# Kernel optimization log

Hardware: AMD Instinct MI355X
Metric: run time of the kernel (lower is better)

## Reference

```python
import jax, jax.numpy as jnp
import numpy as np

# dims: M=512 new tokens, N=2048 model dim, D=128 head dim, H=16 heads,
# L=4096 cache length, P=2048 cache write offset

def setup_inputs() -> dict:
    key = jax.random.key(0)
    k0, k1, k2, k3 = jax.random.split(key, 4)
    M, N, D, L = 512, 2048, 128, 4096
    X = jax.random.normal(k0, (M, N), jnp.float32)
    # scale weights ~1/sqrt(N) so projections have unit-ish scale
    W_qkv = jax.random.normal(k1, (N, 3 * N), jnp.float32) * (N ** -0.5)
    H = N // D
    cache_K = jax.random.normal(k2, (H, L, D), jnp.float32)
    # realistic cache state: keys stored in cache are RMS-normalized
    cache_K = cache_K * jax.lax.rsqrt(jnp.mean(cache_K * cache_K, axis=-1, keepdims=True))
    cache_V = jax.random.normal(k3, (H, L, D), jnp.float32)
    return {"X": X, "W_qkv": W_qkv, "cache_K": cache_K, "cache_V": cache_V, "P": 2048}


def reference(X, W_qkv, cache_K, cache_V, P):
    M = X.shape[0]
    H, L, D = cache_K.shape
    qkv = X @ W_qkv                              # [M, 3N]
    q, k, v = jnp.split(qkv, 3, axis=-1)         # each [M, N]
    q = q.reshape(M, H, D).transpose(1, 0, 2)    # [H, M, D]
    k = k.reshape(M, H, D).transpose(1, 0, 2)
    v = v.reshape(M, H, D).transpose(1, 0, 2)
    # RMS-style normalization (no learned gain, no eps in original)
    q = q * jax.lax.rsqrt(jnp.mean(q * q, axis=-1, keepdims=True))
    k = k * jax.lax.rsqrt(jnp.mean(k * k, axis=-1, keepdims=True))
    # scatter-update into KV cache at position P
    Kc = jax.lax.dynamic_update_slice(cache_K, k, (0, P, 0))  # [H, L, D]
    Vc = jax.lax.dynamic_update_slice(cache_V, v, (0, P, 0))
    # unmasked, unscaled attention over the full cache (faithful to original:
    # plain exp/sum, no max-subtraction, no 1/sqrt(D))
    scores = jnp.einsum('hmd,hld->hml', q, Kc)   # [H, M, L]
    w = jnp.exp(scores)
    w = w / jnp.sum(w, axis=-1, keepdims=True)
    out = jnp.einsum('hml,hld->hmd', w, Vc)      # [H, M, D]
    return out.transpose(1, 0, 2).reshape(M, H * D)
```

## Files before the change

kernel.cpp:

```cpp
#include <hip/hip_runtime.h>
#include <math.h>

typedef _Float16 half_t;
typedef _Float16 half8 __attribute__((ext_vector_type(8)));
typedef _Float16 half4_t __attribute__((ext_vector_type(4)));
typedef _Float16 half2_t __attribute__((ext_vector_type(2)));
typedef float floatx4 __attribute__((ext_vector_type(4)));

#define M_TOK 512
#define N_DIM 2048
#define D_HEAD 128
#define H_HEADS 16
#define L_CACHE 4096
#define THREE_N 6144
#define NCHUNK 8
#define LCHUNK 512

__global__ __launch_bounds__(256) void prep_kernel(const float* __restrict__ W,
                                                   const float* __restrict__ X,
                                                   half_t* __restrict__ W16T,
                                                   half_t* __restrict__ X16) {
    __shared__ half_t tile[64 * 66];
    int b = blockIdx.x;
    int t = threadIdx.x;

    if (b < 3072) {
        int n0 = (b % 96) * 64, k0 = (b / 96) * 64;
        {
            int k = t >> 2, c0 = (t & 3) * 16;
            const float* src = W + (size_t)(k0 + k) * THREE_N + n0 + c0;
            float4 v[4];
#pragma unroll
            for (int j = 0; j < 4; ++j) v[j] = *(const float4*)(src + j * 4);
#pragma unroll
            for (int j = 0; j < 4; ++j) {
                tile[(c0 + j * 4 + 0) * 66 + k] = (half_t)v[j].x;
                tile[(c0 + j * 4 + 1) * 66 + k] = (half_t)v[j].y;
                tile[(c0 + j * 4 + 2) * 66 + k] = (half_t)v[j].z;
                tile[(c0 + j * 4 + 3) * 66 + k] = (half_t)v[j].w;
            }
        }
        __syncthreads();
        {
            int n = t >> 2, kg = (t & 3) * 16;
            half_t* dst = W16T + (size_t)(n0 + n) * N_DIM + k0 + kg;
            *(half8*)(dst) = *(half8*)&tile[n * 66 + kg];
            *(half8*)(dst + 8) = *(half8*)&tile[n * 66 + kg + 8];
        }
        return;
    }
    b -= 3072;
    {
        size_t i = (size_t)b * 2048 + t * 4;
        float4 v0 = *(const float4*)(X + i);
        float4 v1 = *(const float4*)(X + i + 1024);
        half4_t h0 = {(half_t)v0.x, (half_t)v0.y, (half_t)v0.z, (half_t)v0.w};
        half4_t h1 = {(half_t)v1.x, (half_t)v1.y, (half_t)v1.z, (half_t)v1.w};
        *(half4_t*)(X16 + i) = h0;
        *(half4_t*)(X16 + i + 1024) = h1;
    }
}

__global__ __launch_bounds__(256) void mega_kernel(const half_t* __restrict__ X16,
                                                   const half_t* __restrict__ W16T,
                                                   const float* __restrict__ cK,
                                                   const float* __restrict__ cV,
                                                   const int* __restrict__ Pp,
                                                   half_t* __restrict__ Q16,
                                                   half_t* __restrict__ K16,
                                                   half_t* __restrict__ V16T) {
    __shared__ __align__(16) char smem[46592];
    const int t = threadIdx.x;
    int b = blockIdx.x;

    if (b >= 384) {
        b -= 384;
        const int P = *Pp;
        if (b < 4096) {
            int l0 = (b & 255) * 16;
            if (l0 >= P && l0 + 16 <= P + M_TOK) return;
            size_t i = (size_t)b * 2048 + t * 4;
            int r0 = l0 + (t >> 5), r1 = r0 + 8;
            float4 v0 = *(const float4*)(cK + i);
            float4 v1 = *(const float4*)(cK + i + 1024);
            half4_t h0 = {(half_t)v0.x, (half_t)v0.y, (half_t)v0.z, (half_t)v0.w};
            half4_t h1 = {(half_t)v1.x, (half_t)v1.y, (half_t)v1.z, (half_t)v1.w};
            if (r0 < P || r0 >= P + M_TOK) *(half4_t*)(K16 + i) = h0;
            if (r1 < P || r1 >= P + M_TOK) *(half4_t*)(K16 + i + 1024) = h1;
            return;
        }
        b -= 4096;
        {
            int h = b >> 7;
            int rem = b & 127;
            int lt = rem >> 1, dt = rem & 1;
            int l0 = lt * 64, d0 = dt * 64;
            if (l0 >= P && l0 + 64 <= P + M_TOK) return;
            bool overlap = (l0 < P + M_TOK) && (l0 + 64 > P);
            half_t* tile = (half_t*)smem;
            {
                int l = t >> 2, c0 = (t & 3) * 16;
                const float* src = cV + ((size_t)h * L_CACHE + l0 + l) * D_HEAD + d0 + c0;
                float4 v[4];
#pragma unroll
                for (int j = 0; j < 4; ++j) v[j] = *(const float4*)(src + j * 4);
#pragma unroll
                for (int j = 0; j < 4; ++j) {
                    tile[(c0 + j * 4 + 0) * 66 + l] = (half_t)v[j].x;
                    tile[(c0 + j * 4 + 1) * 66 + l] = (half_t)v[j].y;
                    tile[(c0 + j * 4 + 2) * 66 + l] = (half_t)v[j].z;
                    tile[(c0 + j * 4 + 3) * 66 + l] = (half_t)v[j].w;
                }
            }
            __syncthreads();
            {
                int d = t >> 2, lg = (t & 3) * 16;
                half_t* dst = V16T + ((size_t)h * D_HEAD + d0 + d) * L_CACHE + l0 + lg;
                if (!overlap) {
                    *(half8*)(dst) = *(half8*)&tile[d * 66 + lg];
                    *(half8*)(dst + 8) = *(half8*)&tile[d * 66 + lg + 8];
                } else {
#pragma unroll
                    for (int j = 0; j < 16; ++j) {
                        int l = l0 + lg + j;
                        if (l < P || l >= P + M_TOK) dst[j] = tile[d * 66 + lg + j];
                    }
                }
            }
            return;
        }
    }

    half_t* As = (half_t*)smem;
    half_t* Bs = (half_t*)(smem + 9216);
    half_t* Vt = (half_t*)(smem + 27648);
    float* ssb = (float*)(smem + 46080);
    const int wid = t >> 6, lane = t & 63;
    const int quad = lane >> 4, ln = lane & 15;
    const int bx = b % 48, by = b / 48;
    const int m0 = by * 64, n0 = bx * 128;
    const int wm = (wid >> 1) * 32, wn = (wid & 1) * 64;

    floatx4 acc[2][4] = {};

    const int ar = t >> 3, ag = (t & 7) * 8;
    const int br = t >> 3, bg = (t & 7) * 8;

    for (int k0 = 0; k0 < N_DIM; k0 += 64) {
        __syncthreads();
#pragma unroll
        for (int p = 0; p < 2; ++p) {
            int r = ar + p * 32;
            *(half8*)&As[r * 72 + ag] =
                *(const half8*)(X16 + (size_t)(m0 + r) * N_DIM + k0 + ag);
        }
#pragma unroll
        for (int p = 0; p < 4; ++p) {
            int r = br + p * 32;
            *(half8*)&Bs[r * 72 + bg] =
                *(const half8*)(W16T + (size_t)(n0 + r) * N_DIM + k0 + bg);
        }
        __syncthreads();
#pragma unroll
        for (int kt = 0; kt < 2; ++kt) {
            half8 a[2], bb[4];
#pragma unroll
            for (int i = 0; i < 2; ++i)
                a[i] = *(half8*)&As[(wm + i * 16 + ln) * 72 + kt * 32 + quad * 8];
#pragma unroll
            for (int j = 0; j < 4; ++j)
                bb[j] = *(half8*)&Bs[(wn + j * 16 + ln) * 72 + kt * 32 + quad * 8];
#pragma unroll
            for (int i = 0; i < 2; ++i)
#pragma unroll
                for (int j = 0; j < 4; ++j)
                    acc[i][j] = __builtin_amdgcn_mfma_f32_16x16x32_f16(a[i], bb[j], acc[i][j], 0, 0, 0);
        }
    }

    const int seg = bx >> 4, h = bx & 15;
    const int P = *Pp;

    if (seg < 2) {
        float ss[2][4], scale[2][4];
#pragma unroll
        for (int i = 0; i < 2; ++i)
#pragma unroll
            for (int r = 0; r < 4; ++r) {
                float s = 0.f;
#pragma unroll
                for (int j = 0; j < 4; ++j) s += acc[i][j][r] * acc[i][j][r];
#pragma unroll
                for (int msk = 1; msk < 16; msk <<= 1) s += __shfl_xor(s, msk, 64);
                ss[i][r] = s;
            }
        if (ln == 0) {
#pragma unroll
            for (int i = 0; i < 2; ++i)
#pragma unroll
                for (int r = 0; r < 4; ++r)
                    ssb[wid * 32 + i * 16 + quad * 4 + r] = ss[i][r];
        }
        __syncthreads();
#pragma unroll
        for (int i = 0; i < 2; ++i)
#pragma unroll
            for (int r = 0; r < 4; ++r)
                scale[i][r] =
                    rsqrtf((ss[i][r] + ssb[(wid ^ 1) * 32 + i * 16 + quad * 4 + r]) * (1.0f / 128.0f));
#pragma unroll
        for (int i = 0; i < 2; ++i) {
            int mbase = m0 + wm + i * 16 + quad * 4;
#pragma unroll
            for (int j = 0; j < 4; ++j) {
                int col = wn + j * 16 + ln;
#pragma unroll
                for (int r = 0; r < 4; ++r) {
                    int m = mbase + r;
                    half_t val = (half_t)(acc[i][j][r] * scale[i][r]);
                    if (seg == 0)
                        Q16[((size_t)h * M_TOK + m) * D_HEAD + col] = val;
                    else
                        K16[((size_t)h * L_CACHE + P + m) * D_HEAD + col] = val;
                }
            }
        }
    } else {
#pragma unroll
        for (int i = 0; i < 2; ++i) {
            int mbase = wm + i * 16 + quad * 4;
#pragma unroll
            for (int j = 0; j < 4; ++j) {
                int d = wn + j * 16 + ln;
#pragma unroll
                for (int r = 0; r < 4; ++r)
                    Vt[d * 72 + mbase + r] = (half_t)acc[i][j][r];
            }
        }
        __syncthreads();
#pragma unroll
        for (int p = 0; p < 4; ++p) {
            int s = p * 256 + t;
            int d = s >> 3, sg = s & 7;
            *(half8*)(V16T + ((size_t)h * D_HEAD + d) * L_CACHE + P + m0 + sg * 8) =
                *(half8*)&Vt[d * 72 + sg * 8];
        }
    }
}

__global__ __launch_bounds__(256, 4) void attn_partial_kernel(const half_t* __restrict__ Q16,
                                                              const half_t* __restrict__ K16,
                                                              const half_t* __restrict__ V16T,
                                                              half_t* __restrict__ Opart,
                                                              float* __restrict__ mstat,
                                                              float* __restrict__ lstat) {
    __shared__ half_t Ks[64 * 128];
    __shared__ half_t Vs[128 * 64];
    __shared__ half_t Ps[4 * 16 * 64];
    const int t = threadIdx.x, w = t >> 6, lane = t & 63;
    const int quad = lane >> 4, ln = lane & 15;

    const int bid = blockIdx.x;
    const int xcd = bid & 7, slot = bid >> 3;
    const int pair = (xcd << 4) | (slot >> 3);
    const int h = pair & 15, c = pair >> 4, mi = slot & 7;
    const int mb = mi * 64;

    const half_t* Qh = Q16 + (size_t)h * M_TOK * D_HEAD;
    const half_t* Kh = K16 + (size_t)h * L_CACHE * D_HEAD;
    const half_t* Vh = V16T + (size_t)h * D_HEAD * L_CACHE;

    const int m0 = mb + w * 16;
    half8 qf[4];
#pragma unroll
    for (int dt = 0; dt < 4; ++dt)
        qf[dt] = *(const half8*)(Qh + (size_t)(m0 + ln) * D_HEAD + dt * 32 + quad * 8);

    floatx4 oacc[8] = {};
    float mrow = -INFINITY;
    float lrow = 0.f;

    half_t* Pw = Ps + w * (16 * 64);
    const int psw = (ln & 7) << 3;

    const int l0base = c * LCHUNK;
    const int kr = t >> 4, kc = (t & 15) * 8;
    const int vr = t >> 3, vc = (t & 7) * 8;
    const int ksw = (kr & 7) << 3;
    const int vsw = (vr & 7) << 3;

    half8 kreg[4], vreg[4];
#pragma unroll
    for (int p = 0; p < 4; ++p) {
        kreg[p] = *(const half8*)(Kh + (size_t)(l0base + p * 16 + kr) * D_HEAD + kc);
        vreg[p] = *(const half8*)(Vh + (size_t)(p * 32 + vr) * L_CACHE + l0base + vc);
    }

    for (int it = 0; it < LCHUNK / 64; ++it) {
        __syncthreads();
#pragma unroll
        for (int p = 0; p < 4; ++p)
            *(half8*)&Ks[(p * 16 + kr) * 128 + (kc ^ ksw)] = kreg[p];
#pragma unroll
        for (int p = 0; p < 4; ++p)
            *(half8*)&Vs[(p * 32 + vr) * 64 + (vc ^ vsw)] = vreg[p];
        if (it + 1 < LCHUNK / 64) {
            int l1 = l0base + (it + 1) * 64;
#pragma unroll
            for (int p = 0; p < 4; ++p) {
                kreg[p] = *(const half8*)(Kh + (size_t)(l1 + p * 16 + kr) * D_HEAD + kc);
                vreg[p] = *(const half8*)(Vh + (size_t)(p * 32 + vr) * L_CACHE + l1 + vc);
            }
        }
        __syncthreads();

        floatx4 sacc[4] = {};
#pragma unroll
        for (int dt = 0; dt < 4; ++dt) {
            half8 kf[4];
#pragma unroll
            for (int nt = 0; nt < 4; ++nt)
                kf[nt] = *(half8*)&Ks[(nt * 16 + ln) * 128 + ((dt * 32 + quad * 8) ^ psw)];
#pragma unroll
            for (int nt = 0; nt < 4; ++nt)
                sacc[nt] = __builtin_amdgcn_mfma_f32_16x16x32_f16(kf[nt], qf[dt], sacc[nt], 0, 0, 0);
        }

        {
            float mx = sacc[0][0];
#pragma unroll
            for (int nt = 0; nt < 4; ++nt)
#pragma unroll
                for (int r = 0; r < 4; ++r) mx = fmaxf(mx, sacc[nt][r]);
            mx = fmaxf(mx, __shfl_xor(mx, 16));
            mx = fmaxf(mx, __shfl_xor(mx, 32));
            if (__ballot(mx > mrow)) {
                float mnew = fmaxf(mrow, mx);
                float alpha = __expf(mrow - mnew);
                mrow = mnew;
                lrow *= alpha;
                float ar[4];
#pragma unroll
                for (int r = 0; r < 4; ++r) ar[r] = __shfl(alpha, quad * 4 + r, 16);
#pragma unroll
                for (int nt8 = 0; nt8 < 8; ++nt8)
#pragma unroll
                    for (int r = 0; r < 4; ++r) oacc[nt8][r] *= ar[r];
            }
            float psum = 0.f;
#pragma unroll
            for (int nt = 0; nt < 4; ++nt) {
                half4_t h4;
#pragma unroll
                for (int r = 0; r < 4; ++r) {
                    float p = __expf(sacc[nt][r] - mrow);
                    psum += p;
                    h4[r] = (half_t)p;
                }
                *(half4_t*)&Pw[ln * 64 + ((nt * 16 + quad * 4) ^ psw)] = h4;
            }
            psum += __shfl_xor(psum, 16);
            psum += __shfl_xor(psum, 32);
            lrow += psum;
        }

#pragma unroll
        for (int kt = 0; kt < 2; ++kt) {
            half8 a = *(half8*)&Pw[ln * 64 + ((kt * 32 + quad * 8) ^ psw)];
#pragma unroll
            for (int nt8 = 0; nt8 < 8; ++nt8) {
                half8 b = *(half8*)&Vs[(nt8 * 16 + ln) * 64 + ((kt * 32 + quad * 8) ^ psw)];
                oacc[nt8] = __builtin_amdgcn_mfma_f32_16x16x32_f16(a, b, oacc[nt8], 0, 0, 0);
            }
        }
    }

    half_t* Oc = Opart + ((size_t)(c * H_HEADS + h) * M_TOK) * D_HEAD;
    float* ms = mstat + (size_t)(c * H_HEADS + h) * M_TOK;
    float* ls = lstat + (size_t)(c * H_HEADS + h) * M_TOK;
#pragma unroll
    for (int nt8 = 0; nt8 < 8; ++nt8) {
        int col = nt8 * 16 + ln;
#pragma unroll
        for (int r = 0; r < 4; ++r)
            Oc[(size_t)(m0 + quad * 4 + r) * D_HEAD + col] = (half_t)oacc[nt8][r];
    }
    if (lane < 16) {
        ms[m0 + lane] = mrow;
        ls[m0 + lane] = lrow;
    }
}

__global__ __launch_bounds__(256) void combine_kernel(const half_t* __restrict__ Opart,
                                                      const float* __restrict__ mstat,
                                                      const float* __restrict__ lstat,
                                                      float* __restrict__ out) {
    int gw = blockIdx.x * 4 + (threadIdx.x >> 6);
    int lane = threadIdx.x & 63;
    int h = gw >> 9, m = gw & 511;
    int d = lane * 2;

    float ms[NCHUNK];
    float mg = -INFINITY;
#pragma unroll
    for (int c = 0; c < NCHUNK; ++c) {
        ms[c] = mstat[((c * H_HEADS + h) << 9) + m];
        mg = fmaxf(mg, ms[c]);
    }
    float denom = 0.f, o0 = 0.f, o1 = 0.f;
#pragma unroll
    for (int c = 0; c < NCHUNK; ++c) {
        float e = __expf(ms[c] - mg);
        denom += lstat[((c * H_HEADS + h) << 9) + m] * e;
        const half_t* Oc = Opart + (((size_t)(c * H_HEADS + h) << 9) + m) * D_HEAD + d;
        half2_t v = *(const half2_t*)Oc;
        o0 += (float)v.x * e;
        o1 += (float)v.y * e;
    }
    float inv = 1.0f / denom;
    float* op = out + (size_t)m * N_DIM + h * D_HEAD + d;
    op[0] = o0 * inv;
    op[1] = o1 * inv;
}

extern "C" void kernel_launch(void* const* d_in, const int* in_sizes, int n_in,
                              void* d_out, int out_size, void* d_ws, size_t ws_size,
                              hipStream_t stream) {
    const float* X = (const float*)d_in[0];
    const float* W = (const float*)d_in[1];
    const float* cK = (const float*)d_in[2];
    const float* cV = (const float*)d_in[3];
    const int* Pp = (const int*)d_in[4];
    float* out = (float*)d_out;

    char* ws = (char*)d_ws;
    half_t* Q16 = (half_t*)(ws + 0);
    half_t* K16 = (half_t*)(ws + 2097152);
    half_t* V16T = (half_t*)(ws + 18874368);
    half_t* X16 = (half_t*)(ws + 35651584);
    half_t* W16T = (half_t*)(ws + 37748736);
    half_t* Opart = (half_t*)(ws + 37748736);
    float* mstat = (float*)(ws + 71303168);
    float* lstat = (float*)(ws + 71827456);

    prep_kernel<<<3584, 256, 0, stream>>>(W, X, W16T, X16);
    mega_kernel<<<6528, 256, 0, stream>>>(X16, W16T, cK, cV, Pp, Q16, K16, V16T);
    attn_partial_kernel<<<1024, 256, 0, stream>>>(Q16, K16, V16T, Opart, mstat, lstat);
    combine_kernel<<<2048, 256, 0, stream>>>(Opart, mstat, lstat, out);
}
```

Baseline: 212.4 us.

## Fuse split-L combine into attention kernel via last-block atomic counter

Removes the separate combine kernel launch. Each attention block bumps an atomic counter for its (head, m-block) group, and the last of the eight chunk blocks to finish merges all partial outputs and writes the final result. This saves one kernel launch and its tail. In exchange the last-arriving blocks run a serial tail, and a hipMemsetAsync is added to reset the counters.

```diff
diff --git a/kernel.cpp b/kernel.cpp
--- a/kernel.cpp
+++ b/kernel.cpp
@@ -253,10 +253,13 @@
                                                               const half_t* __restrict__ V16T,
                                                               half_t* __restrict__ Opart,
                                                               float* __restrict__ mstat,
-                                                              float* __restrict__ lstat) {
+                                                              float* __restrict__ lstat,
+                                                              float* __restrict__ out,
+                                                              int* __restrict__ cnt) {
     __shared__ half_t Ks[64 * 128];
     __shared__ half_t Vs[128 * 64];
     __shared__ half_t Ps[4 * 16 * 64];
+    __shared__ int lastS;
     const int t = threadIdx.x, w = t >> 6, lane = t & 63;
     const int quad = lane >> 4, ln = lane & 15;
 
@@ -339,13 +342,13 @@
                 float alpha = __expf(mrow - mnew);
                 mrow = mnew;
                 lrow *= alpha;
-                float ar[4];
-#pragma unroll
-                for (int r = 0; r < 4; ++r) ar[r] = __shfl(alpha, quad * 4 + r, 16);
+                float ar4[4];
+#pragma unroll
+                for (int r = 0; r < 4; ++r) ar4[r] = __shfl(alpha, quad * 4 + r, 16);
 #pragma unroll
                 for (int nt8 = 0; nt8 < 8; ++nt8)
 #pragma unroll
-                    for (int r = 0; r < 4; ++r) oacc[nt8][r] *= ar[r];
+                    for (int r = 0; r < 4; ++r) oacc[nt8][r] *= ar4[r];
             }
             float psum = 0.f;
 #pragma unroll
@@ -389,38 +392,49 @@
         ms[m0 + lane] = mrow;
         ls[m0 + lane] = lrow;
     }
-}
-
-__global__ __launch_bounds__(256) void combine_kernel(const half_t* __restrict__ Opart,
-                                                      const float* __restrict__ mstat,
-                                                      const float* __restrict__ lstat,
-                                                      float* __restrict__ out) {
-    int gw = blockIdx.x * 4 + (threadIdx.x >> 6);
-    int lane = threadIdx.x & 63;
-    int h = gw >> 9, m = gw & 511;
-    int d = lane * 2;
-
-    float ms[NCHUNK];
-    float mg = -INFINITY;
-#pragma unroll
-    for (int c = 0; c < NCHUNK; ++c) {
-        ms[c] = mstat[((c * H_HEADS + h) << 9) + m];
-        mg = fmaxf(mg, ms[c]);
-    }
-    float denom = 0.f, o0 = 0.f, o1 = 0.f;
-#pragma unroll
-    for (int c = 0; c < NCHUNK; ++c) {
-        float e = __expf(ms[c] - mg);
-        denom += lstat[((c * H_HEADS + h) << 9) + m] * e;
-        const half_t* Oc = Opart + (((size_t)(c * H_HEADS + h) << 9) + m) * D_HEAD + d;
-        half2_t v = *(const half2_t*)Oc;
-        o0 += (float)v.x * e;
-        o1 += (float)v.y * e;
-    }
-    float inv = 1.0f / denom;
-    float* op = out + (size_t)m * N_DIM + h * D_HEAD + d;
-    op[0] = o0 * inv;
-    op[1] = o1 * inv;
+
+    __syncthreads();
+    if (t == 0) {
+        int prev = __hip_atomic_fetch_add(&cnt[h * 8 + mi], 1, __ATOMIC_ACQ_REL,
+                                          __HIP_MEMORY_SCOPE_AGENT);
+        int last = (prev == NCHUNK - 1) ? 1 : 0;
+        if (last) {
+            __hip_atomic_store(&cnt[h * 8 + mi], 0, __ATOMIC_RELAXED,
+                               __HIP_MEMORY_SCOPE_AGENT);
+            __builtin_amdgcn_fence(__ATOMIC_ACQUIRE, "agent");
+        }
+        lastS = last;
+    }
+    __syncthreads();
+    if (lastS) {
+#pragma unroll 1
+        for (int rr = w; rr < 64; rr += 4) {
+            int m = mb + rr;
+            int d = lane * 2;
+            float msv[NCHUNK];
+            float mg = -INFINITY;
+#pragma unroll
+            for (int cc = 0; cc < NCHUNK; ++cc) {
+                msv[cc] = mstat[((cc * H_HEADS + h) << 9) + m];
+                mg = fmaxf(mg, msv[cc]);
+            }
+            float denom = 0.f, o0 = 0.f, o1 = 0.f;
+#pragma unroll
+            for (int cc = 0; cc < NCHUNK; ++cc) {
+                float e = __expf(msv[cc] - mg);
+                denom += lstat[((cc * H_HEADS + h) << 9) + m] * e;
+                const half_t* Oc2 =
+                    Opart + (((size_t)(cc * H_HEADS + h) << 9) + m) * D_HEAD + d;
+                half2_t v = *(const half2_t*)Oc2;
+                o0 += (float)v.x * e;
+                o1 += (float)v.y * e;
+            }
+            float inv = 1.0f / denom;
+            float* op = out + (size_t)m * N_DIM + h * D_HEAD + d;
+            op[0] = o0 * inv;
+            op[1] = o1 * inv;
+        }
+    }
 }
 
 extern "C" void kernel_launch(void* const* d_in, const int* in_sizes, int n_in,
@@ -442,9 +456,11 @@
     half_t* Opart = (half_t*)(ws + 37748736);
     float* mstat = (float*)(ws + 71303168);
     float* lstat = (float*)(ws + 71827456);
-
+    int* cnt = (int*)(ws + 72089600);
+
+    hipMemsetAsync(cnt, 0, 512, stream);
     prep_kernel<<<3584, 256, 0, stream>>>(W, X, W16T, X16);
     mega_kernel<<<6528, 256, 0, stream>>>(X16, W16T, cK, cV, Pp, Q16, K16, V16T);
-    attn_partial_kernel<<<1024, 256, 0, stream>>>(Q16, K16, V16T, Opart, mstat, lstat);
-    combine_kernel<<<2048, 256, 0, stream>>>(Opart, mstat, lstat, out);
+    attn_partial_kernel<<<1024, 256, 0, stream>>>(Q16, K16, V16T, Opart, mstat,
+                                                  lstat, out, cnt);
 }
```

Result: slower. 263.4 us (+24.0%).
